# Kernel optimization log

Hardware: AMD Instinct MI355X
Metric: run time of the kernel (lower is better)

Reference implementation:

```python
import jax, jax.numpy as jnp
import numpy as np

D_MODEL = 1024
N_HEADS = 16
D_K = D_MODEL // N_HEADS


def setup_inputs() -> dict:
    key = jax.random.key(0)
    ks = jax.random.split(key, 12)
    B, S = 4, 2048
    scale = 1.0 / np.sqrt(D_MODEL)
    inp = {
        "Q_in": jax.random.normal(ks[0], (B, S, D_MODEL), jnp.float32),
        "K_in": jax.random.normal(ks[1], (B, S, D_MODEL), jnp.float32),
        "V_in": jax.random.normal(ks[2], (B, S, D_MODEL), jnp.float32),
        "Wq": jax.random.normal(ks[3], (D_MODEL, D_MODEL), jnp.float32) * scale,
        "bq": jnp.zeros((D_MODEL,), jnp.float32),
        "Wk": jax.random.normal(ks[4], (D_MODEL, D_MODEL), jnp.float32) * scale,
        "bk": jnp.zeros((D_MODEL,), jnp.float32),
        "Wv": jax.random.normal(ks[5], (D_MODEL, D_MODEL), jnp.float32) * scale,
        "bv": jnp.zeros((D_MODEL,), jnp.float32),
        "Wo": jax.random.normal(ks[6], (D_MODEL, D_MODEL), jnp.float32) * scale,
        "bo": jnp.zeros((D_MODEL,), jnp.float32),
    }
    return inp


def reference(Q_in, K_in, V_in, Wq, bq, Wk, bk, Wv, bv, Wo, bo):
    B, S, _ = Q_in.shape
    # QKV projections, split into heads: [B, H, S, d_k]
    def proj(x, W, b):
        y = jnp.einsum('bsd,df->bsf', x, W) + b
        return y.reshape(B, S, N_HEADS, D_K).transpose(0, 2, 1, 3)

    Q = proj(Q_in, Wq, bq)
    K = proj(K_in, Wk, bk)
    V = proj(V_in, Wv, bv)

    # scaled dot-product attention (dropout is identity in eval)
    scores = jnp.einsum('bhqd,bhkd->bhqk', Q, K) / jnp.sqrt(jnp.float32(D_K)).astype(Q.dtype)
    p_attn = jax.nn.softmax(scores, axis=-1)
    x = jnp.einsum('bhqk,bhkd->bhqd', p_attn, V)

    # merge heads and output projection
    x = x.transpose(0, 2, 1, 3).reshape(B, S, D_MODEL)
    return jnp.einsum('bsd,df->bsf', x, Wo) + bo
```

## Files before the change

### kernel.cpp

```cpp
#include <hip/hip_runtime.h>

#define DEV __device__ __forceinline__

typedef _Float16 f16;
typedef __attribute__((ext_vector_type(8))) _Float16 f16x8;
typedef __attribute__((ext_vector_type(4))) _Float16 f16x4;
typedef __attribute__((ext_vector_type(2))) __fp16 fp16v2;
typedef __attribute__((ext_vector_type(4))) float floatx4;

constexpr int DMODEL = 1024;
constexpr int SLEN = 2048;
constexpr float SCALE_Q = 0.125f * 1.4426950408889634f;

DEV void gll16(const void* g, void* lds) {
    __builtin_amdgcn_global_load_lds((const __attribute__((address_space(1))) void*)g,
                                     (__attribute__((address_space(3))) void*)lds, 16, 0, 0);
}

#if __has_builtin(__builtin_amdgcn_exp2f)
DEV float fast_exp2(float x) { return __builtin_amdgcn_exp2f(x); }
#else
DEV float fast_exp2(float x) { return __expf(x * 0.6931471805599453f); }
#endif

DEV unsigned pkh2(float a, float b) {
    union { fp16v2 h; unsigned u; } c;
    c.h = __builtin_amdgcn_cvt_pkrtz(a, b);
    return c.u;
}

#if __has_builtin(__builtin_amdgcn_permlane32_swap) && __has_builtin(__builtin_amdgcn_permlane16_swap)
DEV void pl32swap(unsigned& x, unsigned& y) {
    auto r = __builtin_amdgcn_permlane32_swap(x, y, false, false);
    x = r[0]; y = r[1];
}
DEV void pl16swap(unsigned& x, unsigned& y) {
    auto r = __builtin_amdgcn_permlane16_swap(x, y, false, false);
    x = r[0]; y = r[1];
}
#else
DEV void pl32swap(unsigned& x, unsigned& y) {
    unsigned xs = (unsigned)__shfl_xor((int)x, 32, 64);
    unsigned ys = (unsigned)__shfl_xor((int)y, 32, 64);
    bool lo = (threadIdx.x & 63) < 32;
    unsigned nx = lo ? x : ys, ny = lo ? xs : y;
    x = nx; y = ny;
}
DEV void pl16swap(unsigned& x, unsigned& y) {
    unsigned xs = (unsigned)__shfl_xor((int)x, 16, 64);
    unsigned ys = (unsigned)__shfl_xor((int)y, 16, 64);
    bool ev = (((threadIdx.x & 63) >> 4) & 1) == 0;
    unsigned nx = ev ? x : ys, ny = ev ? xs : y;
    x = nx; y = ny;
}
#endif

DEV f16x8 xform(const floatx4& s0, const floatx4& s1) {
    unsigned X  = pkh2(fast_exp2(s0[0]), fast_exp2(s0[1]));
    unsigned Xp = pkh2(fast_exp2(s0[2]), fast_exp2(s0[3]));
    unsigned Y  = pkh2(fast_exp2(s1[0]), fast_exp2(s1[1]));
    unsigned Yp = pkh2(fast_exp2(s1[2]), fast_exp2(s1[3]));
    pl32swap(X, Y);  pl16swap(X, Y);
    pl32swap(Xp, Yp); pl16swap(Xp, Yp);
    union { unsigned u[4]; f16x8 v; } o;
    o.u[0] = X; o.u[1] = Xp; o.u[2] = Y; o.u[3] = Yp;
    return o.v;
}

__global__ void cvt3(const float* __restrict__ A0, const float* __restrict__ A1,
                     const float* __restrict__ A2, f16* __restrict__ O0,
                     f16* __restrict__ O1, f16* __restrict__ O2) {
    const int seg = blockIdx.x >> 12;
    const int i = (blockIdx.x & 4095) * 256 + threadIdx.x;
    const float* in = seg == 0 ? A0 : seg == 1 ? A1 : A2;
    f16* out = seg == 0 ? O0 : seg == 1 ? O1 : O2;
    const float4 a = ((const float4*)in)[2 * i];
    const float4 b = ((const float4*)in)[2 * i + 1];
    f16x8 h;
    h[0] = (f16)a.x; h[1] = (f16)a.y; h[2] = (f16)a.z; h[3] = (f16)a.w;
    h[4] = (f16)b.x; h[5] = (f16)b.y; h[6] = (f16)b.z; h[7] = (f16)b.w;
    ((f16x8*)out)[i] = h;
}

__global__ void wtrans4(const float* __restrict__ W0, const float* __restrict__ W1,
                        const float* __restrict__ W2, const float* __restrict__ W3,
                        f16* __restrict__ T0, f16* __restrict__ T1,
                        f16* __restrict__ T2, f16* __restrict__ T3) {
    __shared__ float t[32][33];
    const int w = blockIdx.x >> 10, bid = blockIdx.x & 1023;
    const float* W = w == 0 ? W0 : w == 1 ? W1 : w == 2 ? W2 : W3;
    f16* Wt = w == 0 ? T0 : w == 1 ? T1 : w == 2 ? T2 : T3;
    const int tn = bid & 31, tk = bid >> 5;
    const int c = threadIdx.x & 31, r0 = threadIdx.x >> 5;
    for (int i = 0; i < 4; ++i) {
        int r = r0 + i * 8;
        t[r][c] = W[(tk * 32 + r) * DMODEL + tn * 32 + c];
    }
    __syncthreads();
    for (int i = 0; i < 4; ++i) {
        int r = r0 + i * 8;
        Wt[(tn * 32 + r) * DMODEL + tk * 32 + c] = (f16)t[c][r];
    }
}

__global__ __launch_bounds__(256, 2)
void gemm_qkv(const f16* __restrict__ A0, const f16* __restrict__ A1, const f16* __restrict__ A2,
              const f16* __restrict__ B0, const f16* __restrict__ B1, const f16* __restrict__ B2,
              const float* __restrict__ bi0, const float* __restrict__ bi1, const float* __restrict__ bi2,
              f16* __restrict__ C0, f16* __restrict__ C1, f16* __restrict__ C2, int epi_base) {
    __shared__ f16 As[128 * 32];
    __shared__ f16 Bs[128 * 32];
    const int seg = blockIdx.x >> 9, inner = blockIdx.x & 511;
    const int epi = epi_base + seg;
    const f16* A = seg == 0 ? A0 : seg == 1 ? A1 : A2;
    const f16* Bt = seg == 0 ? B0 : seg == 1 ? B1 : B2;
    const float* bias = seg == 0 ? bi0 : seg == 1 ? bi1 : bi2;
    f16* Cp = seg == 0 ? C0 : seg == 1 ? C1 : C2;

    const int tid = threadIdx.x;
    const int wid = tid >> 6, lane = tid & 63;
    const int quad = lane >> 4, l16 = lane & 15;
    const int bm = inner & 63, bn = inner >> 6;
    const int row0 = bm * 128, col0 = bn * 128;
    const int wm = (wid >> 1) * 64, wn = (wid & 1) * 64;

    floatx4 acc[4][4];
    for (int i = 0; i < 4; ++i)
        for (int j = 0; j < 4; ++j) acc[i][j] = {0.f, 0.f, 0.f, 0.f};

    for (int k0 = 0; k0 < DMODEL; k0 += 32) {
        __syncthreads();
        for (int j = 0; j < 2; ++j) {
            int off = (j * 4 + wid) * 1024 + lane * 16;
            int r = off >> 6, cb = (off & 63) >> 1;
            gll16(Bt + (col0 + r) * DMODEL + k0 + cb, (char*)Bs + (j * 4 + wid) * 1024);
            gll16(A + (row0 + r) * DMODEL + k0 + cb, (char*)As + (j * 4 + wid) * 1024);
        }
        __syncthreads();

        f16x8 af[4], bf[4];
        for (int mi = 0; mi < 4; ++mi)
            af[mi] = *(const f16x8*)&As[(wm + mi * 16 + l16) * 32 + quad * 8];
        for (int ni = 0; ni < 4; ++ni)
            bf[ni] = *(const f16x8*)&Bs[(wn + ni * 16 + l16) * 32 + quad * 8];
        for (int mi = 0; mi < 4; ++mi)
            for (int ni = 0; ni < 4; ++ni)
                acc[mi][ni] = __builtin_amdgcn_mfma_f32_16x16x32_f16(af[mi], bf[ni], acc[mi][ni], 0, 0, 0);
    }

    const float scale = (epi == 0) ? SCALE_Q : 1.0f;
    for (int mi = 0; mi < 4; ++mi) {
        for (int ni = 0; ni < 4; ++ni) {
            const int gr0 = row0 + wm + mi * 16 + quad * 4;
            const int gc = col0 + wn + ni * 16 + l16;
            const float bv = bias[gc];
            if (epi == 2) {
                const int b_ = gr0 >> 11, s0 = gr0 & 2047;
                const int h_ = gc >> 6, d_ = gc & 63;
                const int bh = b_ * 16 + h_;
                const int csw = ((s0 >> 3) & 15) ^ (d_ & 7);
                const int s0w = (s0 & ~127) | (csw << 3) | (s0 & 7);
                f16x4 o;
                for (int r = 0; r < 4; ++r) o[r] = (f16)(acc[mi][ni][r] + bv);
                *(f16x4*)&Cp[(bh * 64 + d_) * SLEN + s0w] = o;
            } else {
                for (int r = 0; r < 4; ++r) {
                    const int gr = gr0 + r;
                    const int b_ = gr >> 11, s_ = gr & 2047;
                    const int h_ = gc >> 6, d_ = gc & 63;
                    const int bh = b_ * 16 + h_;
                    const int dsw = (((d_ >> 3) ^ (s_ & 7)) << 3) | (d_ & 7);
                    Cp[(bh * SLEN + s_) * 64 + dsw] = (f16)((acc[mi][ni][r] + bv) * scale);
                }
            }
        }
    }
}

__global__ __launch_bounds__(256, 2)
void gemm_out(const f16* __restrict__ A, const f16* __restrict__ Bt,
              const float* __restrict__ bias, float* __restrict__ Cp) {
    __shared__ f16 As[128 * 32];
    __shared__ f16 Bs[128 * 32];
    const int tid = threadIdx.x;
    const int wid = tid >> 6, lane = tid & 63;
    const int quad = lane >> 4, l16 = lane & 15;
    const int bm = blockIdx.x & 63, bn = blockIdx.x >> 6;
    const int row0 = bm * 128, col0 = bn * 128;
    const int wm = (wid >> 1) * 64, wn = (wid & 1) * 64;

    floatx4 acc[4][4];
    for (int i = 0; i < 4; ++i)
        for (int j = 0; j < 4; ++j) acc[i][j] = {0.f, 0.f, 0.f, 0.f};

    for (int k0 = 0; k0 < DMODEL; k0 += 32) {
        __syncthreads();
        for (int j = 0; j < 2; ++j) {
            int off = (j * 4 + wid) * 1024 + lane * 16;
            int r = off >> 6, cb = (off & 63) >> 1;
            gll16(Bt + (col0 + r) * DMODEL + k0 + cb, (char*)Bs + (j * 4 + wid) * 1024);
            gll16(A + (row0 + r) * DMODEL + k0 + cb, (char*)As + (j * 4 + wid) * 1024);
        }
        __syncthreads();

        f16x8 af[4], bf[4];
        for (int mi = 0; mi < 4; ++mi)
            af[mi] = *(const f16x8*)&As[(wm + mi * 16 + l16) * 32 + quad * 8];
        for (int ni = 0; ni < 4; ++ni)
            bf[ni] = *(const f16x8*)&Bs[(wn + ni * 16 + l16) * 32 + quad * 8];
        for (int mi = 0; mi < 4; ++mi)
            for (int ni = 0; ni < 4; ++ni)
                acc[mi][ni] = __builtin_amdgcn_mfma_f32_16x16x32_f16(af[mi], bf[ni], acc[mi][ni], 0, 0, 0);
    }

    for (int mi = 0; mi < 4; ++mi)
        for (int ni = 0; ni < 4; ++ni) {
            const int gr0 = row0 + wm + mi * 16 + quad * 4;
            const int gc = col0 + wn + ni * 16 + l16;
            const float bv = bias[gc];
            for (int r = 0; r < 4; ++r)
                Cp[(gr0 + r) * DMODEL + gc] = acc[mi][ni][r] + bv;
        }
}

__global__ __launch_bounds__(128, 2)
void flash_k(const f16* __restrict__ Qh, const f16* __restrict__ Kh,
             const f16* __restrict__ Vt, f16* __restrict__ attn) {
    __shared__ f16 smem[16384];
    f16* Qs = smem;
    f16* Ks = smem;
    f16* Vs = smem + 8192;

    const int tid = threadIdx.x;
    const int wid = tid >> 6, lane = tid & 63;
    const int quad = lane >> 4, l16 = lane & 15;
    const int bh = blockIdx.x >> 4, qt = blockIdx.x & 15;
    const int wq = wid * 64;

    const f16* Qbase = Qh + (bh * SLEN + qt * 128) * 64;
#pragma unroll
    for (int j = 0; j < 8; ++j)
        gll16(Qbase + (j * 128 + wid * 64 + lane) * 8, (char*)Qs + (j * 128 + wid * 64) * 16);
    __syncthreads();

    f16x8 qf[4][2];
#pragma unroll
    for (int nq = 0; nq < 4; ++nq)
#pragma unroll
        for (int kc = 0; kc < 2; ++kc)
            qf[nq][kc] = *(const f16x8*)&Qs[(wq + nq * 16 + l16) * 64 +
                                            (((kc * 4 + quad) ^ (l16 & 7)) << 3)];

    floatx4 oacc[4][5];
    for (int nq = 0; nq < 4; ++nq)
        for (int md = 0; md < 5; ++md) oacc[nq][md] = {0.f, 0.f, 0.f, 0.f};

    const f16x8 ones = {(f16)1, (f16)1, (f16)1, (f16)1, (f16)1, (f16)1, (f16)1, (f16)1};
    const f16* Kb = Kh + bh * SLEN * 64;
    const f16* Vb = Vt + bh * 64 * SLEN;

    for (int kv0 = 0; kv0 < SLEN; kv0 += 128) {
        __syncthreads();
#pragma unroll
        for (int j = 0; j < 8; ++j)
            gll16(Kb + kv0 * 64 + (j * 128 + wid * 64 + lane) * 8,
                  (char*)Ks + (j * 128 + wid * 64) * 16);
#pragma unroll
        for (int j = 0; j < 8; ++j) {
            const int ci = j * 128 + wid * 64 + lane;
            const int d_ = ci >> 4, o_ = (ci & 15) * 8;
            gll16(Vb + d_ * SLEN + kv0 + o_, (char*)Vs + (j * 128 + wid * 64) * 16);
        }
        __syncthreads();

#pragma unroll
        for (int c = 0; c < 4; ++c) {
            floatx4 sacc[4][2];
            for (int nq = 0; nq < 4; ++nq)
                for (int t = 0; t < 2; ++t) sacc[nq][t] = {0.f, 0.f, 0.f, 0.f};
#pragma unroll
            for (int t = 0; t < 2; ++t) {
                const int a = c * 2 + t;
#pragma unroll
                for (int kc = 0; kc < 2; ++kc) {
                    f16x8 kf = *(const f16x8*)&Ks[(a * 16 + l16) * 64 +
                                                  (((kc * 4 + quad) ^ (l16 & 7)) << 3)];
                    for (int nq = 0; nq < 4; ++nq)
                        sacc[nq][t] = __builtin_amdgcn_mfma_f32_16x16x32_f16(
                            kf, qf[nq][kc], sacc[nq][t], 0, 0, 0);
                }
            }
            f16x8 pf[4];
#pragma unroll
            for (int nq = 0; nq < 4; ++nq) pf[nq] = xform(sacc[nq][0], sacc[nq][1]);
#pragma unroll
            for (int md = 0; md < 4; ++md) {
                f16x8 vf = *(const f16x8*)&Vs[(md * 16 + l16) * 128 +
                                              (((c * 4 + quad) ^ (l16 & 7)) << 3)];
                for (int nq = 0; nq < 4; ++nq)
                    oacc[nq][md] = __builtin_amdgcn_mfma_f32_16x16x32_f16(
                        vf, pf[nq], oacc[nq][md], 0, 0, 0);
            }
            for (int nq = 0; nq < 4; ++nq)
                oacc[nq][4] = __builtin_amdgcn_mfma_f32_16x16x32_f16(
                    ones, pf[nq], oacc[nq][4], 0, 0, 0);
        }
    }

    const int b_ = bh >> 4, h_ = bh & 15;
#pragma unroll
    for (int nq = 0; nq < 4; ++nq) {
        const float linv = __frcp_rn(oacc[nq][4][0]);
        const int tok = b_ * SLEN + qt * 128 + wq + nq * 16 + l16;
#pragma unroll
        for (int md = 0; md < 4; ++md) {
            f16x4 o;
            for (int r = 0; r < 4; ++r) o[r] = (f16)(oacc[nq][md][r] * linv);
            *(f16x4*)&attn[tok * DMODEL + h_ * 64 + md * 16 + quad * 4] = o;
        }
    }
}

extern "C" void kernel_launch(void* const* d_in, const int* in_sizes, int n_in,
                              void* d_out, int out_size, void* d_ws, size_t ws_size,
                              hipStream_t stream) {
    (void)in_sizes; (void)n_in; (void)out_size;
    const float* Q_in = (const float*)d_in[0];
    const float* K_in = (const float*)d_in[1];
    const float* V_in = (const float*)d_in[2];
    const float* Wq = (const float*)d_in[3];
    const float* bq = (const float*)d_in[4];
    const float* Wk = (const float*)d_in[5];
    const float* bk = (const float*)d_in[6];
    const float* Wv = (const float*)d_in[7];
    const float* bv = (const float*)d_in[8];
    const float* Wo = (const float*)d_in[9];
    const float* bo = (const float*)d_in[10];
    float* out = (float*)d_out;

    char* ws = (char*)d_ws;
    const size_t MB = 1u << 20;
    f16* wtq = (f16*)(ws + 0 * MB);
    f16* wtk = (f16*)(ws + 2 * MB);
    f16* wtv = (f16*)(ws + 4 * MB);
    f16* wto = (f16*)(ws + 6 * MB);
    f16* Qh  = (f16*)(ws + 8 * MB);
    f16* Kh  = (f16*)(ws + 24 * MB);
    f16* Vt  = (f16*)(ws + 40 * MB);
    f16* At  = (f16*)(ws + 56 * MB);

    wtrans4<<<4096, 256, 0, stream>>>(Wq, Wk, Wv, Wo, wtq, wtk, wtv, wto);

    if (ws_size >= 120 * MB) {
        f16* Ac0 = (f16*)(ws + 72 * MB);
        f16* Ac1 = (f16*)(ws + 88 * MB);
        f16* Ac2 = (f16*)(ws + 104 * MB);
        cvt3<<<3 * 4096, 256, 0, stream>>>(Q_in, K_in, V_in, Ac0, Ac1, Ac2);
        gemm_qkv<<<1536, 256, 0, stream>>>(Ac0, Ac1, Ac2, wtq, wtk, wtv,
                                           bq, bk, bv, Qh, Kh, Vt, 0);
    } else {
        f16* Ac = At;
        cvt3<<<4096, 256, 0, stream>>>(Q_in, Q_in, Q_in, Ac, Ac, Ac);
        gemm_qkv<<<512, 256, 0, stream>>>(Ac, Ac, Ac, wtq, wtq, wtq, bq, bq, bq,
                                          Qh, Qh, Qh, 0);
        cvt3<<<4096, 256, 0, stream>>>(K_in, K_in, K_in, Ac, Ac, Ac);
        gemm_qkv<<<512, 256, 0, stream>>>(Ac, Ac, Ac, wtk, wtk, wtk, bk, bk, bk,
                                          Kh, Kh, Kh, 1);
        cvt3<<<4096, 256, 0, stream>>>(V_in, V_in, V_in, Ac, Ac, Ac);
        gemm_qkv<<<512, 256, 0, stream>>>(Ac, Ac, Ac, wtv, wtv, wtv, bv, bv, bv,
                                          Vt, Vt, Vt, 2);
    }

    flash_k<<<1024, 128, 0, stream>>>(Qh, Kh, Vt, At);
    gemm_out<<<512, 256, 0, stream>>>(At, wto, bo, out);
}
```

Baseline: 341.2 us.

## Widen flash kernel to four waves, software-pipeline PV, remap blocks per XCD

The attention kernel now runs 256 threads per block. Each wave owns 32 query rows instead of 64, which halves the per-wave Q fragments and accumulators. The PV MFMA for chunk c-1 is interleaved with the QK MFMA for chunk c so the softmax transform can overlap matrix work. Blocks are remapped so each XCD handles a contiguous set of heads for K/V cache locality, and the GEMM launch-bound occupancy hints are raised to 3. Four waves share each K/V tile, which cuts per-block load work, but register pressure or the new occupancy targets could force spills.

```diff
diff --git a/kernel.cpp b/kernel.cpp
--- a/kernel.cpp
+++ b/kernel.cpp
@@ -103,7 +103,7 @@
     }
 }
 
-__global__ __launch_bounds__(256, 2)
+__global__ __launch_bounds__(256, 3)
 void gemm_qkv(const f16* __restrict__ A0, const f16* __restrict__ A1, const f16* __restrict__ A2,
               const f16* __restrict__ B0, const f16* __restrict__ B1, const f16* __restrict__ B2,
               const float* __restrict__ bi0, const float* __restrict__ bi1, const float* __restrict__ bi2,
@@ -177,7 +177,7 @@
     }
 }
 
-__global__ __launch_bounds__(256, 2)
+__global__ __launch_bounds__(256, 3)
 void gemm_out(const f16* __restrict__ A, const f16* __restrict__ Bt,
               const float* __restrict__ bias, float* __restrict__ Cp) {
     __shared__ f16 As[128 * 32];
@@ -223,7 +223,7 @@
         }
 }
 
-__global__ __launch_bounds__(128, 2)
+__global__ __launch_bounds__(256, 4)
 void flash_k(const f16* __restrict__ Qh, const f16* __restrict__ Kh,
              const f16* __restrict__ Vt, f16* __restrict__ attn) {
     __shared__ f16 smem[16384];
@@ -234,25 +234,28 @@
     const int tid = threadIdx.x;
     const int wid = tid >> 6, lane = tid & 63;
     const int quad = lane >> 4, l16 = lane & 15;
-    const int bh = blockIdx.x >> 4, qt = blockIdx.x & 15;
-    const int wq = wid * 64;
+    const int xcd = blockIdx.x & 7, jj = blockIdx.x >> 3;
+    const int bh = xcd * 8 + (jj & 7), qt = jj >> 3;
+    const int mq = wid * 32;
 
     const f16* Qbase = Qh + (bh * SLEN + qt * 128) * 64;
 #pragma unroll
-    for (int j = 0; j < 8; ++j)
-        gll16(Qbase + (j * 128 + wid * 64 + lane) * 8, (char*)Qs + (j * 128 + wid * 64) * 16);
+    for (int j = 0; j < 4; ++j) {
+        const int ch = j * 4 + wid;
+        gll16(Qbase + ch * 512 + lane * 8, (char*)Qs + ch * 1024);
+    }
     __syncthreads();
 
-    f16x8 qf[4][2];
-#pragma unroll
-    for (int nq = 0; nq < 4; ++nq)
+    f16x8 qf[2][2];
+#pragma unroll
+    for (int nq = 0; nq < 2; ++nq)
 #pragma unroll
         for (int kc = 0; kc < 2; ++kc)
-            qf[nq][kc] = *(const f16x8*)&Qs[(wq + nq * 16 + l16) * 64 +
+            qf[nq][kc] = *(const f16x8*)&Qs[(mq + nq * 16 + l16) * 64 +
                                             (((kc * 4 + quad) ^ (l16 & 7)) << 3)];
 
-    floatx4 oacc[4][5];
-    for (int nq = 0; nq < 4; ++nq)
+    floatx4 oacc[2][5];
+    for (int nq = 0; nq < 2; ++nq)
         for (int md = 0; md < 5; ++md) oacc[nq][md] = {0.f, 0.f, 0.f, 0.f};
 
     const f16x8 ones = {(f16)1, (f16)1, (f16)1, (f16)1, (f16)1, (f16)1, (f16)1, (f16)1};
@@ -262,21 +265,24 @@
     for (int kv0 = 0; kv0 < SLEN; kv0 += 128) {
         __syncthreads();
 #pragma unroll
-        for (int j = 0; j < 8; ++j)
-            gll16(Kb + kv0 * 64 + (j * 128 + wid * 64 + lane) * 8,
-                  (char*)Ks + (j * 128 + wid * 64) * 16);
-#pragma unroll
-        for (int j = 0; j < 8; ++j) {
-            const int ci = j * 128 + wid * 64 + lane;
+        for (int j = 0; j < 4; ++j) {
+            const int ch = j * 4 + wid;
+            gll16(Kb + kv0 * 64 + ch * 512 + lane * 8, (char*)Ks + ch * 1024);
+        }
+#pragma unroll
+        for (int j = 0; j < 4; ++j) {
+            const int ch = j * 4 + wid;
+            const int ci = ch * 64 + lane;
             const int d_ = ci >> 4, o_ = (ci & 15) * 8;
-            gll16(Vb + d_ * SLEN + kv0 + o_, (char*)Vs + (j * 128 + wid * 64) * 16);
-        }
-        __syncthreads();
-
+            gll16(Vb + d_ * SLEN + kv0 + o_, (char*)Vs + ch * 1024);
+        }
+        __syncthreads();
+
+        f16x8 pf[2];
 #pragma unroll
         for (int c = 0; c < 4; ++c) {
-            floatx4 sacc[4][2];
-            for (int nq = 0; nq < 4; ++nq)
+            floatx4 sacc[2][2];
+            for (int nq = 0; nq < 2; ++nq)
                 for (int t = 0; t < 2; ++t) sacc[nq][t] = {0.f, 0.f, 0.f, 0.f};
 #pragma unroll
             for (int t = 0; t < 2; ++t) {
@@ -285,33 +291,46 @@
                 for (int kc = 0; kc < 2; ++kc) {
                     f16x8 kf = *(const f16x8*)&Ks[(a * 16 + l16) * 64 +
                                                   (((kc * 4 + quad) ^ (l16 & 7)) << 3)];
-                    for (int nq = 0; nq < 4; ++nq)
+                    for (int nq = 0; nq < 2; ++nq)
                         sacc[nq][t] = __builtin_amdgcn_mfma_f32_16x16x32_f16(
                             kf, qf[nq][kc], sacc[nq][t], 0, 0, 0);
                 }
             }
-            f16x8 pf[4];
-#pragma unroll
-            for (int nq = 0; nq < 4; ++nq) pf[nq] = xform(sacc[nq][0], sacc[nq][1]);
-#pragma unroll
-            for (int md = 0; md < 4; ++md) {
-                f16x8 vf = *(const f16x8*)&Vs[(md * 16 + l16) * 128 +
-                                              (((c * 4 + quad) ^ (l16 & 7)) << 3)];
-                for (int nq = 0; nq < 4; ++nq)
-                    oacc[nq][md] = __builtin_amdgcn_mfma_f32_16x16x32_f16(
-                        vf, pf[nq], oacc[nq][md], 0, 0, 0);
+            if (c > 0) {
+                const int cp = c - 1;
+#pragma unroll
+                for (int md = 0; md < 4; ++md) {
+                    f16x8 vf = *(const f16x8*)&Vs[(md * 16 + l16) * 128 +
+                                                  (((cp * 4 + quad) ^ (l16 & 7)) << 3)];
+                    for (int nq = 0; nq < 2; ++nq)
+                        oacc[nq][md] = __builtin_amdgcn_mfma_f32_16x16x32_f16(
+                            vf, pf[nq], oacc[nq][md], 0, 0, 0);
+                }
+                for (int nq = 0; nq < 2; ++nq)
+                    oacc[nq][4] = __builtin_amdgcn_mfma_f32_16x16x32_f16(
+                        ones, pf[nq], oacc[nq][4], 0, 0, 0);
             }
-            for (int nq = 0; nq < 4; ++nq)
-                oacc[nq][4] = __builtin_amdgcn_mfma_f32_16x16x32_f16(
-                    ones, pf[nq], oacc[nq][4], 0, 0, 0);
-        }
+#pragma unroll
+            for (int nq = 0; nq < 2; ++nq) pf[nq] = xform(sacc[nq][0], sacc[nq][1]);
+        }
+#pragma unroll
+        for (int md = 0; md < 4; ++md) {
+            f16x8 vf = *(const f16x8*)&Vs[(md * 16 + l16) * 128 +
+                                          (((3 * 4 + quad) ^ (l16 & 7)) << 3)];
+            for (int nq = 0; nq < 2; ++nq)
+                oacc[nq][md] = __builtin_amdgcn_mfma_f32_16x16x32_f16(
+                    vf, pf[nq], oacc[nq][md], 0, 0, 0);
+        }
+        for (int nq = 0; nq < 2; ++nq)
+            oacc[nq][4] = __builtin_amdgcn_mfma_f32_16x16x32_f16(
+                ones, pf[nq], oacc[nq][4], 0, 0, 0);
     }
 
     const int b_ = bh >> 4, h_ = bh & 15;
 #pragma unroll
-    for (int nq = 0; nq < 4; ++nq) {
+    for (int nq = 0; nq < 2; ++nq) {
         const float linv = __frcp_rn(oacc[nq][4][0]);
-        const int tok = b_ * SLEN + qt * 128 + wq + nq * 16 + l16;
+        const int tok = b_ * SLEN + qt * 128 + mq + nq * 16 + l16;
 #pragma unroll
         for (int md = 0; md < 4; ++md) {
             f16x4 o;
@@ -371,6 +390,6 @@
                                           Vt, Vt, Vt, 2);
     }
 
-    flash_k<<<1024, 128, 0, stream>>>(Qh, Kh, Vt, At);
+    flash_k<<<1024, 256, 0, stream>>>(Qh, Kh, Vt, At);
     gemm_out<<<512, 256, 0, stream>>>(At, wto, bo, out);
 }
```

Result: slower. 348.6 us (+2.2%).
